# Kernel optimization log

Hardware: AMD Instinct MI355X
Metric: run time of the kernel (lower is better)

Reference implementation:

```python
import jax, jax.numpy as jnp
import numpy as np
import math

B, S, D = 2, 2048, 2048
H, KVH, HD = 16, 8, 128  # n_heads, n_kv_heads, head_dim
N_REP = H // KVH
ROPE_THETA = 500000.0
NEG_INF = -1e9


def _rope(t, f):
    # t: (B,S,nh,HD) viewed as pairs; f: (S,HD//2,2) = (cos,sin)
    tp = t.reshape(*t.shape[:-1], HD // 2, 2)          # (B,S,nh,HD//2,2)
    fb = f[:, None]                                     # (S,1,HD//2,2)
    row1 = (tp * fb).sum(-1)                            # x0*c + x1*s
    f_rot = jnp.stack([fb[..., 1], -fb[..., 0]], axis=-1)  # (s, -c)
    row0 = (tp * f_rot).sum(-1)                         # x0*s - x1*c
    return jnp.stack([row0, row1], axis=-1).reshape(t.shape)


def setup_inputs() -> dict:
    key = jax.random.key(0)
    ks = jax.random.split(key, 5)
    x = jax.random.normal(ks[0], (B, S, D), dtype=jnp.float32)
    # RoPE table: (S, HD//2, 2) stacked (cos, sin)
    inv_freq = 1.0 / (ROPE_THETA ** (np.arange(0, HD, 2, dtype=np.float32) / HD))
    t = np.arange(S, dtype=np.float32)
    ang = np.outer(t, inv_freq)                         # (S, HD//2)
    freqs_cis = jnp.asarray(np.stack([np.cos(ang), np.sin(ang)], axis=-1))
    # causal additive mask (S,S)
    mask = jnp.where(jnp.triu(jnp.ones((S, S), dtype=bool), k=1), NEG_INF, 0.0).astype(jnp.float32)
    sc = 1.0 / math.sqrt(D)
    wq = jax.random.normal(ks[1], (D, H * HD), dtype=jnp.float32) * sc
    wk = jax.random.normal(ks[2], (D, KVH * HD), dtype=jnp.float32) * sc
    wv = jax.random.normal(ks[3], (D, KVH * HD), dtype=jnp.float32) * sc
    wo = jax.random.normal(ks[4], (H * HD, D), dtype=jnp.float32) * sc
    return {"x": x, "freqs_cis": freqs_cis, "mask": mask, "wq": wq, "wk": wk, "wv": wv, "wo": wo}


def reference(x, freqs_cis, mask, wq, wk, wv, wo):
    bsz, seqlen, _ = x.shape
    xq = (x @ wq).reshape(bsz, seqlen, H, HD)
    xk = (x @ wk).reshape(bsz, seqlen, KVH, HD)
    xv = (x @ wv).reshape(bsz, seqlen, KVH, HD)
    xq = _rope(xq, freqs_cis)
    xk = _rope(xk, freqs_cis)
    keys = jnp.repeat(xk, N_REP, axis=2)                # (B,S,H,HD)
    values = jnp.repeat(xv, N_REP, axis=2)
    q = xq.transpose(0, 2, 1, 3)                        # (B,H,S,HD)
    k = keys.transpose(0, 2, 1, 3)
    v = values.transpose(0, 2, 1, 3)
    scores = jnp.einsum('bhqd,bhkd->bhqk', q, k) / math.sqrt(HD)
    scores = scores + mask                              # broadcast (S,S)
    probs = jax.nn.softmax(scores.astype(jnp.float32), axis=-1).astype(q.dtype)
    out = jnp.einsum('bhqk,bhkd->bhqd', probs, v)
    out = out.transpose(0, 2, 1, 3).reshape(bsz, seqlen, H * HD)
    return out @ wo
```

## Files before the change

kernel.cpp:

```cpp
#include <hip/hip_runtime.h>

typedef short short8 __attribute__((ext_vector_type(8)));
typedef float v4f __attribute__((ext_vector_type(4)));

#define LOG2E 1.4426950408889634f

__device__ __forceinline__ unsigned short f2bf(float f) {
  unsigned int u = __float_as_uint(f);
  u += 0x7fff + ((u >> 16) & 1);
  return (unsigned short)(u >> 16);
}
__device__ __forceinline__ float b2f(unsigned short h) {
  return __uint_as_float(((unsigned int)h) << 16);
}
__device__ __forceinline__ void gl_lds16(const void* g, void* l) {
  __builtin_amdgcn_global_load_lds((const __attribute__((address_space(1))) void*)g,
                                   (__attribute__((address_space(3))) void*)l, 16, 0, 0);
}

__global__ __launch_bounds__(256) void cvt_f32_bf16(const float* __restrict__ src,
                                                    unsigned short* __restrict__ dst, int n) {
  int i = (blockIdx.x * 256 + threadIdx.x) * 4;
  if (i < n) {
    float4 v = *(const float4*)(src + i);
    ushort4 o;
    o.x = f2bf(v.x); o.y = f2bf(v.y); o.z = f2bf(v.z); o.w = f2bf(v.w);
    *(ushort4*)(dst + i) = o;
  }
}

__global__ __launch_bounds__(256) void transpose_f32_bf16(const float* __restrict__ src,
                                                          unsigned short* __restrict__ dst,
                                                          int srcCols) {
  __shared__ float tile[64][65];
  const int c0 = blockIdx.x * 64;
  const int r0 = blockIdx.y * 64;
  const int t = threadIdx.x;
#pragma unroll
  for (int i = 0; i < 16; ++i) {
    int idx = t + i * 256; int r = idx >> 6, c = idx & 63;
    tile[r][c] = src[(size_t)(r0 + r) * srcCols + c0 + c];
  }
  __syncthreads();
#pragma unroll
  for (int i = 0; i < 16; ++i) {
    int idx = t + i * 256; int r = idx >> 6, c = idx & 63;
    dst[(size_t)(c0 + r) * 2048 + r0 + c] = f2bf(tile[c][r]);
  }
}

template <bool OUT_BF16>
__global__ __launch_bounds__(256) void gemm_bt(const unsigned short* __restrict__ A,
                                               const unsigned short* __restrict__ Bt,
                                               void* __restrict__ Cv,
                                               int M, int N, int K) {
  __shared__ __align__(16) unsigned short As[2][128 * 32];
  __shared__ __align__(16) unsigned short Bs[2][128 * 32];
  const int t = threadIdx.x;
  const int wave = t >> 6, lane = t & 63, quad = lane >> 4, l16 = lane & 15;
  const int tm = blockIdx.y * 128, tn = blockIdx.x * 128;
  const int wm = (wave >> 1) * 64, wn = (wave & 1) * 64;
  v4f acc[4][4];
#pragma unroll
  for (int i = 0; i < 4; ++i)
#pragma unroll
    for (int j = 0; j < 4; ++j) acc[i][j] = (v4f){0.f, 0.f, 0.f, 0.f};

  const int swz = (l16 >> 1) & 3;

  const int s0 = t, s1 = 256 + t;
  const unsigned short* pa0 = A + (size_t)(tm + (s0 >> 2)) * K + ((s0 & 3) ^ ((s0 >> 3) & 3)) * 8;
  const unsigned short* pa1 = A + (size_t)(tm + (s1 >> 2)) * K + ((s1 & 3) ^ ((s1 >> 3) & 3)) * 8;
  const unsigned short* pb0 = Bt + (size_t)(tn + (s0 >> 2)) * K + ((s0 & 3) ^ ((s0 >> 3) & 3)) * 8;
  const unsigned short* pb1 = Bt + (size_t)(tn + (s1 >> 2)) * K + ((s1 & 3) ^ ((s1 >> 3) & 3)) * 8;
  const int dOff0 = (wave * 64) * 8;
  const int dOff1 = (256 + wave * 64) * 8;

  gl_lds16(pa0, &As[0][dOff0]); gl_lds16(pa1, &As[0][dOff1]);
  gl_lds16(pb0, &Bs[0][dOff0]); gl_lds16(pb1, &Bs[0][dOff1]);
  pa0 += 32; pa1 += 32; pb0 += 32; pb1 += 32;

  const int nit = K >> 5;
  for (int it = 0; it < nit; ++it) {
    __syncthreads();
    const int cur = it & 1;
    if (it + 1 < nit) {
      const int nxt = cur ^ 1;
      gl_lds16(pa0, &As[nxt][dOff0]); gl_lds16(pa1, &As[nxt][dOff1]);
      gl_lds16(pb0, &Bs[nxt][dOff0]); gl_lds16(pb1, &Bs[nxt][dOff1]);
      pa0 += 32; pa1 += 32; pb0 += 32; pb1 += 32;
    }
    short8 af[4], bf[4];
#pragma unroll
    for (int mt = 0; mt < 4; ++mt)
      af[mt] = *(const short8*)(&As[cur][(wm + mt * 16 + l16) * 32 + (quad ^ swz) * 8]);
#pragma unroll
    for (int nt = 0; nt < 4; ++nt)
      bf[nt] = *(const short8*)(&Bs[cur][(wn + nt * 16 + l16) * 32 + (quad ^ swz) * 8]);
#pragma unroll
    for (int mt = 0; mt < 4; ++mt)
#pragma unroll
      for (int nt = 0; nt < 4; ++nt)
        acc[mt][nt] = __builtin_amdgcn_mfma_f32_16x16x32_bf16(af[mt], bf[nt], acc[mt][nt], 0, 0, 0);
  }

#pragma unroll
  for (int mt = 0; mt < 4; ++mt)
#pragma unroll
    for (int nt = 0; nt < 4; ++nt)
#pragma unroll
      for (int r = 0; r < 4; ++r) {
        int row = tm + wm + mt * 16 + quad * 4 + r;
        int col = tn + wn + nt * 16 + l16;
        float v = acc[mt][nt][r];
        if (OUT_BF16) ((unsigned short*)Cv)[(size_t)row * N + col] = f2bf(v);
        else          ((float*)Cv)[(size_t)row * N + col] = v;
      }
}

template <bool OUT_BF16>
__global__ __launch_bounds__(512, 2) void gemm256(const unsigned short* __restrict__ A,
                                                  const unsigned short* __restrict__ Bt,
                                                  void* __restrict__ Cv,
                                                  int M, int N, int K) {
  __shared__ __align__(16) unsigned short As[2][256 * 64];
  __shared__ __align__(16) unsigned short Bs[2][256 * 64];
  const int t = threadIdx.x;
  const int wave = t >> 6, lane = t & 63, quad = lane >> 4, l16 = lane & 15;
  const int wr = wave >> 2, wc = wave & 3;

  const int gx = N >> 8;
  int id = blockIdx.y * gridDim.x + blockIdx.x;
  const int nwg = gridDim.x * gridDim.y;
  id = (id & 7) * (nwg >> 3) + (id >> 3);
  const int tm = (id / gx) << 8, tn = (id % gx) << 8;

  v4f acc[8][4];
#pragma unroll
  for (int i = 0; i < 8; ++i)
#pragma unroll
    for (int j = 0; j < 4; ++j) acc[i][j] = (v4f){0.f, 0.f, 0.f, 0.f};

  const int s0 = t, s1 = 512 + t;
  const size_t hA = (size_t)128 * K;
  const unsigned short* a0 = A + (size_t)(tm + (s0 >> 3)) * K + ((s0 & 7) ^ ((s0 >> 3) & 7)) * 8;
  const unsigned short* a1 = A + (size_t)(tm + (s1 >> 3)) * K + ((s1 & 7) ^ ((s1 >> 3) & 7)) * 8;
  const unsigned short* b0 = Bt + (size_t)(tn + (s0 >> 3)) * K + ((s0 & 7) ^ ((s0 >> 3) & 7)) * 8;
  const unsigned short* b1 = Bt + (size_t)(tn + (s1 >> 3)) * K + ((s1 & 7) ^ ((s1 >> 3) & 7)) * 8;
  const int d0 = (wave * 64) * 8;
  const int d1 = (512 + wave * 64) * 8;

#define STG_A(buf, h, koff)                                         \
  do {                                                              \
    gl_lds16(a0 + (size_t)(h) * hA + (koff), &As[buf][(h) * 8192 + d0]); \
    gl_lds16(a1 + (size_t)(h) * hA + (koff), &As[buf][(h) * 8192 + d1]); \
  } while (0)
#define STG_B(buf, h, koff)                                         \
  do {                                                              \
    gl_lds16(b0 + (size_t)(h) * hA + (koff), &Bs[buf][(h) * 8192 + d0]); \
    gl_lds16(b1 + (size_t)(h) * hA + (koff), &Bs[buf][(h) * 8192 + d1]); \
  } while (0)

  const int aBase = (wr * 128 + l16) * 64;
  const int bBase = (wc * 64 + l16) * 64;
  const int c0 = (quad ^ (l16 & 7)) * 8;
  const int c1 = ((4 + quad) ^ (l16 & 7)) * 8;

  const int nkt = K >> 6;

  STG_A(0, 0, 0); STG_A(0, 1, 0);
  STG_B(0, 0, 0); STG_B(0, 1, 0);
  STG_B(1, 0, 64); STG_A(1, 0, 64);
  asm volatile("s_waitcnt vmcnt(4)" ::: "memory");
  __builtin_amdgcn_s_barrier();

  short8 af[4][2], bf[4][2];
  for (int kt = 0; kt < nkt; ++kt) {
    const int cur = kt & 1, nxt = cur ^ 1;
    const int koff = kt << 6;

#pragma unroll
    for (int m = 0; m < 4; ++m) {
      af[m][0] = *(const short8*)(&As[cur][aBase + m * 1024 + c0]);
      af[m][1] = *(const short8*)(&As[cur][aBase + m * 1024 + c1]);
    }
#pragma unroll
    for (int n = 0; n < 2; ++n) {
      bf[n][0] = *(const short8*)(&Bs[cur][bBase + n * 1024 + c0]);
      bf[n][1] = *(const short8*)(&Bs[cur][bBase + n * 1024 + c1]);
    }
    if (kt + 1 < nkt) { STG_A(nxt, 1, koff + 64); STG_B(nxt, 1, koff + 64); }
    __builtin_amdgcn_s_barrier();
    asm volatile("s_waitcnt lgkmcnt(0)" ::: "memory");
    __builtin_amdgcn_s_setprio(1);
#pragma unroll
    for (int m = 0; m < 4; ++m)
#pragma unroll
      for (int n = 0; n < 2; ++n) {
        acc[m][n] = __builtin_amdgcn_mfma_f32_16x16x32_bf16(af[m][0], bf[n][0], acc[m][n], 0, 0, 0);
        acc[m][n] = __builtin_amdgcn_mfma_f32_16x16x32_bf16(af[m][1], bf[n][1], acc[m][n], 0, 0, 0);
      }
    __builtin_amdgcn_s_setprio(0);
    __builtin_amdgcn_s_barrier();

#pragma unroll
    for (int n = 2; n < 4; ++n) {
      bf[n][0] = *(const short8*)(&Bs[cur][bBase + n * 1024 + c0]);
      bf[n][1] = *(const short8*)(&Bs[cur][bBase + n * 1024 + c1]);
    }
    __builtin_amdgcn_s_barrier();
    asm volatile("s_waitcnt lgkmcnt(0)" ::: "memory");
    __builtin_amdgcn_s_setprio(1);
#pragma unroll
    for (int m = 0; m < 4; ++m)
#pragma unroll
      for (int n = 2; n < 4; ++n) {
        acc[m][n] = __builtin_amdgcn_mfma_f32_16x16x32_bf16(af[m][0], bf[n][0], acc[m][n], 0, 0, 0);
        acc[m][n] = __builtin_amdgcn_mfma_f32_16x16x32_bf16(af[m][1], bf[n][1], acc[m][n], 0, 0, 0);
      }
    __builtin_amdgcn_s_setprio(0);
    __builtin_amdgcn_s_barrier();

#pragma unroll
    for (int m = 0; m < 4; ++m) {
      af[m][0] = *(const short8*)(&As[cur][aBase + (4 + m) * 1024 + c0]);
      af[m][1] = *(const short8*)(&As[cur][aBase + (4 + m) * 1024 + c1]);
    }
    if (kt + 2 < nkt) STG_B(cur, 0, koff + 128);
    __builtin_amdgcn_s_barrier();
    asm volatile("s_waitcnt lgkmcnt(0)" ::: "memory");
    __builtin_amdgcn_s_setprio(1);
#pragma unroll
    for (int m = 0; m < 4; ++m)
#pragma unroll
      for (int n = 0; n < 2; ++n) {
        acc[4 + m][n] = __builtin_amdgcn_mfma_f32_16x16x32_bf16(af[m][0], bf[n][0], acc[4 + m][n], 0, 0, 0);
        acc[4 + m][n] = __builtin_amdgcn_mfma_f32_16x16x32_bf16(af[m][1], bf[n][1], acc[4 + m][n], 0, 0, 0);
      }
    __builtin_amdgcn_s_setprio(0);
    __builtin_amdgcn_s_barrier();

    if (kt + 2 < nkt) {
      STG_A(cur, 0, koff + 128);
      asm volatile("s_waitcnt vmcnt(4)" ::: "memory");
    } else {
      asm volatile("s_waitcnt vmcnt(0)" ::: "memory");
    }
    __builtin_amdgcn_s_barrier();
    __builtin_amdgcn_s_setprio(1);
#pragma unroll
    for (int m = 0; m < 4; ++m)
#pragma unroll
      for (int n = 2; n < 4; ++n) {
        acc[4 + m][n] = __builtin_amdgcn_mfma_f32_16x16x32_bf16(af[m][0], bf[n][0], acc[4 + m][n], 0, 0, 0);
        acc[4 + m][n] = __builtin_amdgcn_mfma_f32_16x16x32_bf16(af[m][1], bf[n][1], acc[4 + m][n], 0, 0, 0);
      }
    __builtin_amdgcn_s_setprio(0);
    __builtin_amdgcn_s_barrier();
  }
#undef STG_A
#undef STG_B

#pragma unroll
  for (int mf = 0; mf < 8; ++mf)
#pragma unroll
    for (int nf = 0; nf < 4; ++nf)
#pragma unroll
      for (int r = 0; r < 4; ++r) {
        int row = tm + wr * 128 + mf * 16 + quad * 4 + r;
        int col = tn + wc * 64 + nf * 16 + l16;
        float v = acc[mf][nf][r];
        if (OUT_BF16) ((unsigned short*)Cv)[(size_t)row * N + col] = f2bf(v);
        else          ((float*)Cv)[(size_t)row * N + col] = v;
      }
}

__global__ __launch_bounds__(256) void rope_k(unsigned short* __restrict__ qkv,
                                              const float* __restrict__ freqs) {
  const int bs = blockIdx.x;
  const int s = bs & 2047;
  const float qscale = 0.08838834764831845f;
  unsigned int* row = (unsigned int*)(qkv + (size_t)bs * 4096);
  const float2* fr2 = (const float2*)(freqs + s * 128);
#pragma unroll
  for (int k = 0; k < 6; ++k) {
    int d = threadIdx.x + k * 256;
    float sc = (d < 1024) ? qscale : 1.0f;
    float2 cs = fr2[d & 63];
    unsigned int w = row[d];
    float x0 = b2f((unsigned short)(w & 0xffffu));
    float x1 = b2f((unsigned short)(w >> 16));
    float y0 = (x0 * cs.y - x1 * cs.x) * sc;
    float y1 = (x0 * cs.x + x1 * cs.y) * sc;
    row[d] = ((unsigned int)f2bf(y1) << 16) | (unsigned int)f2bf(y0);
  }
}

__global__ __launch_bounds__(256) void transpose_v(const unsigned short* __restrict__ qkv,
                                                   unsigned short* __restrict__ vt) {
  __shared__ unsigned short tile[64][65];
  const int s0 = blockIdx.x * 64, d0 = blockIdx.y * 64;
  const int bk = blockIdx.z; const int b = bk >> 3, kv = bk & 7;
  const int t = threadIdx.x;
#pragma unroll
  for (int i = 0; i < 16; ++i) {
    int idx = t + i * 256; int r = idx >> 6, c = idx & 63;
    tile[r][c] = qkv[(size_t)(b * 2048 + s0 + r) * 4096 + 3072 + kv * 128 + d0 + c];
  }
  __syncthreads();
#pragma unroll
  for (int i = 0; i < 16; ++i) {
    int idx = t + i * 256; int r = idx >> 6, c = idx & 63;
    vt[((size_t)bk * 128 + d0 + r) * 2048 + s0 + c] = tile[c][r];
  }
}

__global__ __launch_bounds__(256) void attn_k(const unsigned short* __restrict__ qkv,
                                              const unsigned short* __restrict__ vt,
                                              unsigned short* __restrict__ Ob) {
  __shared__ __align__(16) unsigned short Ks[64 * 128];
  __shared__ __align__(16) unsigned short Vs[128 * 64];
  __shared__ __align__(16) unsigned short Ps[4][16 * 64];
  const int t = threadIdx.x, wave = t >> 6, lane = t & 63, quad = lane >> 4, l16 = lane & 15;
  const int jpair = blockIdx.x, h = blockIdx.y, b = blockIdx.z;
  const int kv = h >> 1;

  for (int pass = 0; pass < 2; ++pass) {
    const int qblk = (pass == 0) ? jpair : 31 - jpair;
    const int q0 = qblk * 64;

    short8 qf[4];
    {
      const unsigned short* qp =
          qkv + (size_t)(b * 2048 + q0 + wave * 16 + l16) * 4096 + h * 128 + quad * 8;
#pragma unroll
      for (int kc = 0; kc < 4; ++kc) qf[kc] = *(const short8*)(qp + kc * 32);
    }
    v4f oa[8];
#pragma unroll
    for (int i = 0; i < 8; ++i) oa[i] = (v4f){0.f, 0.f, 0.f, 0.f};
    float m_s = -3.0e38f, l_s = 0.f;

    for (int jt = 0; jt <= qblk; ++jt) {
      __syncthreads();
#pragma unroll
      for (int issue = 0; issue < 4; ++issue) {
        int s = issue * 256 + t;
        gl_lds16(qkv + (size_t)(b * 2048 + jt * 64 + (s >> 4)) * 4096 + 2048 + kv * 128 +
                     (((s & 15) ^ ((s >> 4) & 15)) * 8),
                 Ks + (issue * 256 + wave * 64) * 8);
        gl_lds16(vt + ((size_t)(b * 8 + kv) * 128 + (s >> 3)) * 2048 + jt * 64 +
                     (((s & 7) ^ ((s >> 3) & 7)) * 8),
                 Vs + (issue * 256 + wave * 64) * 8);
      }
      __syncthreads();

      v4f st[4];
#pragma unroll
      for (int mt = 0; mt < 4; ++mt) st[mt] = (v4f){0.f, 0.f, 0.f, 0.f};
#pragma unroll
      for (int kc = 0; kc < 4; ++kc)
#pragma unroll
        for (int mt = 0; mt < 4; ++mt) {
          short8 kf = *(const short8*)(Ks + (mt * 16 + l16) * 128 + (((kc * 4 + quad) ^ l16) * 8));
          st[mt] = __builtin_amdgcn_mfma_f32_16x16x32_bf16(kf, qf[kc], st[mt], 0, 0, 0);
        }

      const bool diag = (jt == qblk);
      float mx = -3.0e38f;
#pragma unroll
      for (int mt = 0; mt < 4; ++mt)
#pragma unroll
        for (int r = 0; r < 4; ++r) {
          float v = st[mt][r];
          if (diag && (mt * 16 + quad * 4 + r > wave * 16 + l16)) v = -1.0e30f;
          st[mt][r] = v;
          mx = fmaxf(mx, v);
        }
      mx = fmaxf(mx, __shfl_xor(mx, 16));
      mx = fmaxf(mx, __shfl_xor(mx, 32));
      float mn = fmaxf(m_s, mx);
      float alpha = exp2f((m_s - mn) * LOG2E);
      m_s = mn;
      float lt = 0.f;
#pragma unroll
      for (int mt = 0; mt < 4; ++mt)
#pragma unroll
        for (int r = 0; r < 4; ++r) {
          float p = exp2f((st[mt][r] - mn) * LOG2E);
          st[mt][r] = p;
          lt += p;
        }
      lt += __shfl_xor(lt, 16);
      lt += __shfl_xor(lt, 32);
      l_s = l_s * alpha + lt;

      float a_q[4];
#pragma unroll
      for (int r = 0; r < 4; ++r) a_q[r] = __shfl(alpha, quad * 4 + r);
#pragma unroll
      for (int nt = 0; nt < 8; ++nt)
#pragma unroll
        for (int r = 0; r < 4; ++r) oa[nt][r] *= a_q[r];

#pragma unroll
      for (int mt = 0; mt < 4; ++mt) {
        int pcp = ((mt * 2 + (quad >> 1)) ^ (l16 & 7));
        ushort4 w;
        w.x = f2bf(st[mt][0]); w.y = f2bf(st[mt][1]);
        w.z = f2bf(st[mt][2]); w.w = f2bf(st[mt][3]);
        *(ushort4*)(&Ps[wave][l16 * 64 + pcp * 8 + (quad & 1) * 4]) = w;
      }
      asm volatile("s_waitcnt lgkmcnt(0)" ::: "memory");

      short8 pf[2];
#pragma unroll
      for (int kc2 = 0; kc2 < 2; ++kc2)
        pf[kc2] = *(const short8*)(&Ps[wave][l16 * 64 + (((kc2 * 4 + quad) ^ (l16 & 7)) * 8)]);
#pragma unroll
      for (int nt = 0; nt < 8; ++nt)
#pragma unroll
        for (int kc2 = 0; kc2 < 2; ++kc2) {
          short8 vf = *(const short8*)(Vs + (nt * 16 + l16) * 64 +
                                       (((kc2 * 4 + quad) ^ (l16 & 7)) * 8));
          oa[nt] = __builtin_amdgcn_mfma_f32_16x16x32_bf16(pf[kc2], vf, oa[nt], 0, 0, 0);
        }
    }

    float inv[4];
#pragma unroll
    for (int r = 0; r < 4; ++r) inv[r] = 1.0f / __shfl(l_s, quad * 4 + r);
#pragma unroll
    for (int r = 0; r < 4; ++r) {
      int row = b * 2048 + q0 + wave * 16 + quad * 4 + r;
#pragma unroll
      for (int nt = 0; nt < 8; ++nt)
        Ob[(size_t)row * 2048 + h * 128 + nt * 16 + l16] = f2bf(oa[nt][r] * inv[r]);
    }
    __syncthreads();
  }
}

extern "C" void kernel_launch(void* const* d_in, const int* in_sizes, int n_in,
                              void* d_out, int out_size, void* d_ws, size_t ws_size,
                              hipStream_t stream) {
  (void)in_sizes; (void)n_in; (void)out_size; (void)ws_size;
  const float* x  = (const float*)d_in[0];
  const float* fr = (const float*)d_in[1];
  const float* wq = (const float*)d_in[3];
  const float* wk = (const float*)d_in[4];
  const float* wv = (const float*)d_in[5];
  const float* wo = (const float*)d_in[6];
  float* out = (float*)d_out;

  char* ws = (char*)d_ws;
  unsigned short* Xb    = (unsigned short*)(ws);
  unsigned short* WqkvT = (unsigned short*)(ws + (size_t)(16u << 20));
  unsigned short* WoT   = (unsigned short*)(ws + (size_t)(32u << 20));
  unsigned short* QKV   = (unsigned short*)(ws + (size_t)(40u << 20));
  unsigned short* Vt    = (unsigned short*)(ws);
  unsigned short* Ob    = (unsigned short*)(ws + (size_t)(16u << 20));

  cvt_f32_bf16<<<8192, 256, 0, stream>>>(x, Xb, 2 * 2048 * 2048);
  transpose_f32_bf16<<<dim3(32, 32), 256, 0, stream>>>(wq, WqkvT, 2048);
  transpose_f32_bf16<<<dim3(16, 32), 256, 0, stream>>>(wk, WqkvT + (size_t)2048 * 2048, 1024);
  transpose_f32_bf16<<<dim3(16, 32), 256, 0, stream>>>(wv, WqkvT + (size_t)3072 * 2048, 1024);
  transpose_f32_bf16<<<dim3(32, 32), 256, 0, stream>>>(wo, WoT, 2048);
  gemm256<true><<<dim3(16, 16), 512, 0, stream>>>(Xb, WqkvT, QKV, 4096, 4096, 2048);
  rope_k<<<4096, 256, 0, stream>>>(QKV, fr);
  transpose_v<<<dim3(32, 2, 16), 256, 0, stream>>>(QKV, Vt);
  attn_k<<<dim3(16, 16, 2), 256, 0, stream>>>(QKV, Vt, Ob);
  gemm_bt<false><<<dim3(16, 32), 256, 0, stream>>>(Ob, WoT, out, 4096, 2048, 2048);
}
```

Measured before the change: 364.0 us.

## Double-buffer K/V tiles in attention and skip rescale when max is stable

The attention kernel now double-buffers its K and V LDS tiles, issuing the asynchronous global-to-LDS loads for the next key block before computing on the current one, and syncs through vmcnt waits plus raw barriers. It also adds a lazy online-softmax rescale: the accumulator and running sum are rescaled only when some lane's block max exceeds the running max by more than 8. Masking is split into separate diagonal and off-diagonal paths. The point is to hide memory latency behind MFMA work and cut per-tile exp and multiply work, at the cost of doubling K/V LDS use (possibly lowering occupancy) and allowing unnormalised exponent growth of up to 2^8-ish, which fp32 absorbs.

```diff
diff --git a/kernel.cpp b/kernel.cpp
--- a/kernel.cpp
+++ b/kernel.cpp
@@ -318,16 +318,31 @@
 __global__ __launch_bounds__(256) void attn_k(const unsigned short* __restrict__ qkv,
                                               const unsigned short* __restrict__ vt,
                                               unsigned short* __restrict__ Ob) {
-  __shared__ __align__(16) unsigned short Ks[64 * 128];
-  __shared__ __align__(16) unsigned short Vs[128 * 64];
+  __shared__ __align__(16) unsigned short Ks[2][64 * 128];
+  __shared__ __align__(16) unsigned short Vs[2][128 * 64];
   __shared__ __align__(16) unsigned short Ps[4][16 * 64];
   const int t = threadIdx.x, wave = t >> 6, lane = t & 63, quad = lane >> 4, l16 = lane & 15;
   const int jpair = blockIdx.x, h = blockIdx.y, b = blockIdx.z;
   const int kv = h >> 1;
 
+  auto stage = [&](int jt, int buf) {
+#pragma unroll
+    for (int issue = 0; issue < 4; ++issue) {
+      int s = issue * 256 + t;
+      gl_lds16(qkv + (size_t)(b * 2048 + jt * 64 + (s >> 4)) * 4096 + 2048 + kv * 128 +
+                   (((s & 15) ^ ((s >> 4) & 15)) * 8),
+               &Ks[buf][(issue * 256 + wave * 64) * 8]);
+      gl_lds16(vt + ((size_t)(b * 8 + kv) * 128 + (s >> 3)) * 2048 + jt * 64 +
+                   (((s & 7) ^ ((s >> 3) & 7)) * 8),
+               &Vs[buf][(issue * 256 + wave * 64) * 8]);
+    }
+  };
+
   for (int pass = 0; pass < 2; ++pass) {
     const int qblk = (pass == 0) ? jpair : 31 - jpair;
     const int q0 = qblk * 64;
+
+    stage(0, 0);
 
     short8 qf[4];
     {
@@ -342,18 +357,14 @@
     float m_s = -3.0e38f, l_s = 0.f;
 
     for (int jt = 0; jt <= qblk; ++jt) {
-      __syncthreads();
-#pragma unroll
-      for (int issue = 0; issue < 4; ++issue) {
-        int s = issue * 256 + t;
-        gl_lds16(qkv + (size_t)(b * 2048 + jt * 64 + (s >> 4)) * 4096 + 2048 + kv * 128 +
-                     (((s & 15) ^ ((s >> 4) & 15)) * 8),
-                 Ks + (issue * 256 + wave * 64) * 8);
-        gl_lds16(vt + ((size_t)(b * 8 + kv) * 128 + (s >> 3)) * 2048 + jt * 64 +
-                     (((s & 7) ^ ((s >> 3) & 7)) * 8),
-                 Vs + (issue * 256 + wave * 64) * 8);
-      }
-      __syncthreads();
+      const int cur = jt & 1;
+      if (jt < qblk) {
+        stage(jt + 1, cur ^ 1);
+        asm volatile("s_waitcnt vmcnt(8)" ::: "memory");
+      } else {
+        asm volatile("s_waitcnt vmcnt(0)" ::: "memory");
+      }
+      __builtin_amdgcn_s_barrier();
 
       v4f st[4];
 #pragma unroll
@@ -362,46 +373,56 @@
       for (int kc = 0; kc < 4; ++kc)
 #pragma unroll
         for (int mt = 0; mt < 4; ++mt) {
-          short8 kf = *(const short8*)(Ks + (mt * 16 + l16) * 128 + (((kc * 4 + quad) ^ l16) * 8));
+          short8 kf =
+              *(const short8*)(&Ks[cur][(mt * 16 + l16) * 128 + (((kc * 4 + quad) ^ l16) * 8)]);
           st[mt] = __builtin_amdgcn_mfma_f32_16x16x32_bf16(kf, qf[kc], st[mt], 0, 0, 0);
         }
 
-      const bool diag = (jt == qblk);
       float mx = -3.0e38f;
-#pragma unroll
-      for (int mt = 0; mt < 4; ++mt)
-#pragma unroll
-        for (int r = 0; r < 4; ++r) {
-          float v = st[mt][r];
-          if (diag && (mt * 16 + quad * 4 + r > wave * 16 + l16)) v = -1.0e30f;
-          st[mt][r] = v;
-          mx = fmaxf(mx, v);
-        }
+      if (jt == qblk) {
+#pragma unroll
+        for (int mt = 0; mt < 4; ++mt)
+#pragma unroll
+          for (int r = 0; r < 4; ++r) {
+            float v = st[mt][r];
+            if (mt * 16 + quad * 4 + r > wave * 16 + l16) v = -1.0e30f;
+            st[mt][r] = v;
+            mx = fmaxf(mx, v);
+          }
+      } else {
+#pragma unroll
+        for (int mt = 0; mt < 4; ++mt)
+#pragma unroll
+          for (int r = 0; r < 4; ++r) mx = fmaxf(mx, st[mt][r]);
+      }
       mx = fmaxf(mx, __shfl_xor(mx, 16));
       mx = fmaxf(mx, __shfl_xor(mx, 32));
-      float mn = fmaxf(m_s, mx);
-      float alpha = exp2f((m_s - mn) * LOG2E);
-      m_s = mn;
+
+      if (__ballot(mx > m_s + 8.0f)) {
+        float mn = fmaxf(m_s, mx);
+        float alpha = exp2f((m_s - mn) * LOG2E);
+        m_s = mn;
+        float a_q[4];
+#pragma unroll
+        for (int r = 0; r < 4; ++r) a_q[r] = __shfl(alpha, quad * 4 + r);
+#pragma unroll
+        for (int nt = 0; nt < 8; ++nt)
+#pragma unroll
+          for (int r = 0; r < 4; ++r) oa[nt][r] *= a_q[r];
+        l_s *= alpha;
+      }
       float lt = 0.f;
 #pragma unroll
       for (int mt = 0; mt < 4; ++mt)
 #pragma unroll
         for (int r = 0; r < 4; ++r) {
-          float p = exp2f((st[mt][r] - mn) * LOG2E);
+          float p = exp2f((st[mt][r] - m_s) * LOG2E);
           st[mt][r] = p;
           lt += p;
         }
       lt += __shfl_xor(lt, 16);
       lt += __shfl_xor(lt, 32);
-      l_s = l_s * alpha + lt;
-
-      float a_q[4];
-#pragma unroll
-      for (int r = 0; r < 4; ++r) a_q[r] = __shfl(alpha, quad * 4 + r);
-#pragma unroll
-      for (int nt = 0; nt < 8; ++nt)
-#pragma unroll
-        for (int r = 0; r < 4; ++r) oa[nt][r] *= a_q[r];
+      l_s += lt;
 
 #pragma unroll
       for (int mt = 0; mt < 4; ++mt) {
@@ -421,10 +442,11 @@
       for (int nt = 0; nt < 8; ++nt)
 #pragma unroll
         for (int kc2 = 0; kc2 < 2; ++kc2) {
-          short8 vf = *(const short8*)(Vs + (nt * 16 + l16) * 64 +
-                                       (((kc2 * 4 + quad) ^ (l16 & 7)) * 8));
+          short8 vf = *(const short8*)(&Vs[cur][(nt * 16 + l16) * 64 +
+                                                (((kc2 * 4 + quad) ^ (l16 & 7)) * 8)]);
           oa[nt] = __builtin_amdgcn_mfma_f32_16x16x32_bf16(pf[kc2], vf, oa[nt], 0, 0, 0);
         }
+      __builtin_amdgcn_s_barrier();
     }
 
     float inv[4];
```

New measurement: 351.6 us. 3.4% less time.
